# Kernel tuning notes

Hardware: AMD Instinct MI355X
Metric: run time of the kernel (lower is better)

Reference implementation:

```python
import jax, jax.numpy as jnp
import numpy as np

D_MODEL = 512
N_HEADS = 8
D_HEAD = D_MODEL // N_HEADS
N_BINS = 32


def setup_inputs() -> dict:
    key = jax.random.key(0)
    ks = jax.random.split(key, 12)
    B, N = 8, 1024
    x = jax.random.normal(ks[0], (B, N, D_MODEL), dtype=jnp.float32)
    positions = jax.random.randint(ks[1], (B, N), 0, 5000, dtype=jnp.int32)
    mask = jnp.ones((B, N), dtype=jnp.float32)
    s = 0.02
    qw = jax.random.normal(ks[2], (D_MODEL, D_MODEL), jnp.float32) * s
    qb = jnp.zeros((D_MODEL,), jnp.float32)
    kw = jax.random.normal(ks[3], (D_MODEL, D_MODEL), jnp.float32) * s
    kb = jnp.zeros((D_MODEL,), jnp.float32)
    vw = jax.random.normal(ks[4], (D_MODEL, D_MODEL), jnp.float32) * s
    vb = jnp.zeros((D_MODEL,), jnp.float32)
    ow = jax.random.normal(ks[5], (D_MODEL, D_MODEL), jnp.float32) * s
    ob = jnp.zeros((D_MODEL,), jnp.float32)
    dist_emb = jax.random.normal(ks[6], (N_BINS, N_HEADS), jnp.float32) * s
    order_bias = jnp.zeros((N_HEADS,), jnp.float32)
    bin_edges = jnp.logspace(0.0, 3.0, N_BINS - 1, dtype=jnp.float32)
    return {"x": x, "positions": positions, "mask": mask,
            "qw": qw, "qb": qb, "kw": kw, "kb": kb, "vw": vw, "vb": vb,
            "ow": ow, "ob": ob, "dist_emb": dist_emb, "order_bias": order_bias,
            "bin_edges": bin_edges}


def reference(x, positions, mask, qw, qb, kw, kb, vw, vb, ow, ob, dist_emb, order_bias, bin_edges):
    B, N, _ = x.shape
    scale = jnp.sqrt(jnp.float32(D_HEAD))
    # projections (torch Linear: y = x @ W^T + b), split heads -> (B,H,N,Dh)
    q = (x @ qw.T + qb).reshape(B, N, N_HEADS, D_HEAD).transpose(0, 2, 1, 3)
    k = (x @ kw.T + kb).reshape(B, N, N_HEADS, D_HEAD).transpose(0, 2, 1, 3)
    v = (x @ vw.T + vb).reshape(B, N, N_HEADS, D_HEAD).transpose(0, 2, 1, 3)
    scores = jnp.einsum('bhqd,bhkd->bhqk', q, k) / scale  # (B,H,N,N)
    pos = positions.astype(jnp.float32)
    pos_i = pos[:, :, None]   # (B,N,1)
    pos_j = pos[:, None, :]   # (B,1,N)
    dist = jnp.abs(pos_j - pos_i)  # (B,N,N)
    # torch.bucketize(right=False) == searchsorted side='left'
    bins = jnp.clip(jnp.searchsorted(bin_edges, dist, side='left'), 0, N_BINS - 1)
    dist_bias = dist_emb[bins]  # (B,N,N,H)
    scores = scores + dist_bias.transpose(0, 3, 1, 2)
    order_sign = (pos_j > pos_i).astype(scores.dtype) - 0.5  # (B,N,N)
    scores = scores + order_sign[:, None, :, :] * order_bias[None, :, None, None]
    mask_2d = mask[:, None, None, :] * mask[:, None, :, None]  # (B,1,N,N)
    scores = jnp.where(mask_2d == 0, jnp.float32(-1e9), scores)
    attn = jax.nn.softmax(scores, axis=-1)
    attn = jnp.nan_to_num(attn, nan=0.0)
    out = jnp.einsum('bhqk,bhkd->bhqd', attn, v)
    out = out.transpose(0, 2, 1, 3).reshape(B, N, D_MODEL)
    out = out * mask[..., None]
    return out @ ow.T + ob
```

## Files before the change

### kernel.cpp

```cpp
#include <hip/hip_runtime.h>
#include <hip/hip_bf16.h>

#define SEQ   1024
#define NH    8
#define DH    64

typedef __attribute__((ext_vector_type(8))) _Float16 half8;
typedef __attribute__((ext_vector_type(4))) _Float16 half4;
typedef __attribute__((ext_vector_type(4))) float    f32x4;

#if __has_builtin(__builtin_amdgcn_exp2f)
#define EXP2F __builtin_amdgcn_exp2f
#else
#define EXP2F exp2f
#endif

__device__ inline unsigned pk2(float a, float b) {
  return __builtin_bit_cast(unsigned, __builtin_amdgcn_cvt_pkrtz(a, b));
}
__device__ inline void swap32(unsigned &a, unsigned &b) {
  asm("v_permlane32_swap_b32 %0, %1" : "+v"(a), "+v"(b));
}
__device__ inline void swap16(unsigned &a, unsigned &b) {
  asm("v_permlane16_swap_b32 %0, %1" : "+v"(a), "+v"(b));
}
__device__ inline half8 mk8(unsigned a, unsigned b, unsigned c, unsigned d) {
  union { unsigned u[4]; half8 h; } x;
  x.u[0] = a; x.u[1] = b; x.u[2] = c; x.u[3] = d;
  return x.h;
}
__device__ __forceinline__ void gload16(const _Float16* g, _Float16* l) {
  __builtin_amdgcn_global_load_lds((const __attribute__((address_space(1))) void*)g,
                                   (__attribute__((address_space(3))) void*)l, 16, 0, 0);
}

#define BARRIER1 do {                                        \
    __builtin_amdgcn_sched_barrier(0);                       \
    asm volatile("s_waitcnt vmcnt(1)" ::: "memory");         \
    __builtin_amdgcn_s_barrier();                            \
    __builtin_amdgcn_sched_barrier(0);                       \
  } while (0)

__global__ void prep_all(const float* __restrict__ x,
                         const float* __restrict__ qw, const float* __restrict__ kw,
                         const float* __restrict__ vw, const float* __restrict__ ow,
                         const float* __restrict__ qb, const float* __restrict__ kb,
                         const float* __restrict__ vb, const float* __restrict__ edges,
                         _Float16* __restrict__ xh, _Float16* __restrict__ wqkvh,
                         _Float16* __restrict__ owh, float* __restrict__ qkvbias,
                         unsigned char* __restrict__ lutd) {
  const int blk = blockIdx.x, tid = threadIdx.x;
  if (blk < 4096) {
    int g = blk * 256 + tid;
    float4 v = reinterpret_cast<const float4*>(x)[g];
    half4 u;
    u[0] = (_Float16)v.x; u[1] = (_Float16)v.y; u[2] = (_Float16)v.z; u[3] = (_Float16)v.w;
    reinterpret_cast<half4*>(xh)[g] = u;
  } else if (blk < 5122) {
    int g = (blk - 4096) * 256 + tid;
    if (g < 196608) {
      const float* src = (g < 65536) ? qw : (g < 131072) ? kw : vw;
      int lg = g & 65535;
      float4 v = reinterpret_cast<const float4*>(src)[lg];
      half4 u;
      u[0] = (_Float16)v.x; u[1] = (_Float16)v.y; u[2] = (_Float16)v.z; u[3] = (_Float16)v.w;
      reinterpret_cast<half4*>(wqkvh)[g] = u;
    } else if (g < 262144) {
      int lg = g - 196608;
      float4 v = reinterpret_cast<const float4*>(ow)[lg];
      half4 u;
      u[0] = (_Float16)v.x; u[1] = (_Float16)v.y; u[2] = (_Float16)v.z; u[3] = (_Float16)v.w;
      reinterpret_cast<half4*>(owh)[lg] = u;
    } else if (g < 262528) {
      int lg = g - 262144;
      const float* src = (lg < 128) ? qb : (lg < 256) ? kb : vb;
      int ll = lg & 127;
      reinterpret_cast<float4*>(qkvbias)[lg] = reinterpret_cast<const float4*>(src)[ll];
    }
  } else {
    int d = (blk - 5122) * 256 + tid;
    float fd = (float)d;
    int bin = 0;
#pragma unroll
    for (int t = 0; t < 31; ++t) bin += (edges[t] < fd) ? 1 : 0;
    lutd[d] = (unsigned char)bin;
  }
}

__global__ __launch_bounds__(256) void prep_ebins(const int* __restrict__ positions,
                                                  const float* __restrict__ mask,
                                                  const unsigned char* __restrict__ lutd,
                                                  unsigned char* __restrict__ ebins) {
  __shared__ unsigned char lutl[5120];
  __shared__ int posl[SEQ];
  __shared__ unsigned char mk[SEQ];
  const int b = blockIdx.x >> 8, j0 = (blockIdx.x & 255) * 4;
  const int tid = threadIdx.x;
  for (int i = tid; i < 1280; i += 256)
    reinterpret_cast<unsigned*>(lutl)[i] = reinterpret_cast<const unsigned*>(lutd)[i];
  for (int i = tid; i < SEQ; i += 256) {
    posl[i] = positions[b * SEQ + i];
    mk[i] = (mask[b * SEQ + i] == 0.f) ? 32 : 0;
  }
  __syncthreads();
  const int c0 = tid * 4;
  const int widx = (tid >> 4) * 16 + (tid & 3) * 4 + ((tid >> 2) & 3);
#pragma unroll
  for (int jj = 0; jj < 4; ++jj) {
    const int j = j0 + jj;
    const int pr = posl[j];
    unsigned out = 0;
#pragma unroll
    for (int r = 0; r < 4; ++r) {
      int c = c0 + r;
      int pc = posl[c];
      int d = pc - pr; d = d < 0 ? -d : d;
      if (d > 5119) d = 5119;
      unsigned e = lutl[d] | (unsigned)mk[c] | ((pc > pr) ? 64u : 0u);
      out |= e << (8 * r);
    }
    reinterpret_cast<unsigned*>(&ebins[(size_t)(b * SEQ + j) * SEQ])[widx] = out;
  }
}

__global__ __launch_bounds__(256) void qkv_gemm3(const _Float16* __restrict__ xh,
                                                 const _Float16* __restrict__ wh,
                                                 const float* __restrict__ bias,
                                                 _Float16* __restrict__ qkv) {
  __shared__ __attribute__((aligned(16))) _Float16 As[128 * 64];
  __shared__ __attribute__((aligned(16))) _Float16 Bs[128 * 64];
  const int m0 = blockIdx.x * 128, n0 = blockIdx.y * 128;
  const int tid = threadIdx.x, w = tid >> 6, lane = tid & 63;
  const int lr = lane & 15, lg = lane >> 4;
  const int wr = (w >> 1) * 64, wc = (w & 1) * 64;
  f32x4 acc[4][4] = {};
  const int srow8 = lane >> 3;
  const int scol = ((lane & 7) ^ srow8) * 8;
  for (int k0 = 0; k0 < 512; k0 += 64) {
#pragma unroll
    for (int j = 0; j < 4; ++j) {
      const int row = (w * 4 + j) * 8 + srow8;
      gload16(&xh[(size_t)(m0 + row) * 512 + k0 + scol], &As[(w * 4 + j) * 512]);
      gload16(&wh[(size_t)(n0 + row) * 512 + k0 + scol], &Bs[(w * 4 + j) * 512]);
    }
    __syncthreads();
#pragma unroll
    for (int kk = 0; kk < 2; ++kk) {
      half8 af[4], bf[4];
#pragma unroll
      for (int mt = 0; mt < 4; ++mt) {
        const int row = wr + mt * 16 + lr;
        af[mt] = *reinterpret_cast<const half8*>(
            (const char*)As + row * 128 + (((kk * 4 + lg) ^ (row & 7)) * 16));
      }
#pragma unroll
      for (int nt = 0; nt < 4; ++nt) {
        const int row = wc + nt * 16 + lr;
        bf[nt] = *reinterpret_cast<const half8*>(
            (const char*)Bs + row * 128 + (((kk * 4 + lg) ^ (row & 7)) * 16));
      }
#pragma unroll
      for (int mt = 0; mt < 4; ++mt)
#pragma unroll
        for (int nt = 0; nt < 4; ++nt)
          acc[mt][nt] = __builtin_amdgcn_mfma_f32_16x16x32_f16(af[mt], bf[nt], acc[mt][nt], 0, 0, 0);
    }
    __syncthreads();
  }
  const int p = n0 >> 9;
  const float scl = (p == 0) ? 0.125f : (p == 1) ? 1.44269504f : 1.0f;
  if (p < 2) {
#pragma unroll
    for (int nt = 0; nt < 4; ++nt) {
      int n = n0 + wc + nt * 16 + lr;
      float bv = bias[n];
      int c = n & 511, h = c >> 6, d = c & 63;
#pragma unroll
      for (int mt = 0; mt < 4; ++mt)
#pragma unroll
        for (int r = 0; r < 4; ++r) {
          int m = m0 + wr + mt * 16 + lg * 4 + r;
          int bb = m >> 10, nn = m & 1023;
          qkv[p * 4194304 + ((bb * NH + h) * SEQ + nn) * DH + d] = (_Float16)((acc[mt][nt][r] + bv) * scl);
        }
    }
  } else {
#pragma unroll
    for (int nt = 0; nt < 4; ++nt) {
      int n = n0 + wc + nt * 16 + lr;
      float bv = bias[n];
      int c = n & 511, h = c >> 6, d = c & 63;
#pragma unroll
      for (int mt = 0; mt < 4; ++mt) {
        int m = m0 + wr + mt * 16 + lg * 4;
        int bb = m >> 10, nn = m & 1023;
        half4 st;
#pragma unroll
        for (int r = 0; r < 4; ++r) st[r] = (_Float16)(acc[mt][nt][r] + bv);
        *reinterpret_cast<half4*>(&qkv[8388608 + ((bb * NH + h) * DH + d) * SEQ + nn]) = st;
      }
    }
  }
}

#define ASTAGE(bufi, kv0_) do {                                                              \
    _Pragma("unroll") for (int j = 0; j < 2; ++j) {                                          \
      const int row_ = (w * 2 + j) * 8 + (lane >> 3);                                        \
      const int c_ = ((lane & 7) ^ (row_ & 7)) * 8;                                          \
      gload16(Kg + (size_t)((kv0_) + row_) * 64 + c_, &KsL + (bufi) * 4096 + (w * 2 + j) * 512); \
      gload16(Vtg + (size_t)row_ * 1024 + (kv0_) + c_, &VtL + (bufi) * 4096 + (w * 2 + j) * 512); \
    }                                                                                        \
  } while (0)

#define EBL(dst, kt_) do {                                                                   \
    uint4 e4_ = *reinterpret_cast<const uint4*>(ebrow + (kt_) * 64);                         \
    dst[0] = e4_.x; dst[1] = e4_.y; dst[2] = e4_.z; dst[3] = e4_.w;                          \
  } while (0)

#define ACOMP(bufi, ebw) do {                                                                \
    f32x4 s[4];                                                                              \
    _Pragma("unroll") for (int ct = 0; ct < 4; ++ct) {                                       \
      const unsigned eb_ = ebw[ct];                                                          \
      s[ct][0] = elut3[eb_ & 127u];                                                          \
      s[ct][1] = elut3[(eb_ >> 8) & 127u];                                                   \
      s[ct][2] = elut3[(eb_ >> 16) & 127u];                                                  \
      s[ct][3] = elut3[(eb_ >> 24) & 127u];                                                  \
    }                                                                                        \
    __builtin_amdgcn_s_setprio(1);                                                           \
    _Pragma("unroll") for (int ct = 0; ct < 4; ++ct) {                                       \
      half8 kf0 = *reinterpret_cast<const half8*>(ksbase + (bufi) * 8192 + koff[ct * 2 + 0]); \
      half8 kf1 = *reinterpret_cast<const half8*>(ksbase + (bufi) * 8192 + koff[ct * 2 + 1]); \
      s[ct] = __builtin_amdgcn_mfma_f32_16x16x32_f16(kf0, qf[0], s[ct], 0, 0, 0);            \
      s[ct] = __builtin_amdgcn_mfma_f32_16x16x32_f16(kf1, qf[1], s[ct], 0, 0, 0);            \
    }                                                                                        \
    __builtin_amdgcn_s_setprio(0);                                                           \
                 \
    unsigned W[4][2];                                                                        \
    _Pragma("unroll") for (int ct = 0; ct < 4; ++ct) {                                       \
      float p0 = EXP2F(s[ct][0]), p1 = EXP2F(s[ct][1]);                                      \
      float p2 = EXP2F(s[ct][2]), p3 = EXP2F(s[ct][3]);                                      \
      l_run += (p0 + p1) + (p2 + p3);                                                        \
      W[ct][0] = pk2(p0, p1);                                                                \
      W[ct][1] = pk2(p2, p3);                                                                \
    }                                                                                        \
    swap32(W[0][0], W[1][0]); swap32(W[0][1], W[1][1]);                                      \
    swap32(W[2][0], W[3][0]); swap32(W[2][1], W[3][1]);                                      \
    swap16(W[0][0], W[1][0]); swap16(W[0][1], W[1][1]);                                      \
    swap16(W[2][0], W[3][0]); swap16(W[2][1], W[3][1]);                                      \
    __builtin_amdgcn_s_setprio(1);                                                           \
    _Pragma("unroll") for (int ks = 0; ks < 2; ++ks) {                                       \
      half8 pa = mk8(W[ks * 2][0], W[ks * 2][1], W[ks * 2 + 1][0], W[ks * 2 + 1][1]);        \
      _Pragma("unroll") for (int dt = 0; dt < 4; ++dt) {                                     \
        half8 vf = *reinterpret_cast<const half8*>(vtbase + (bufi) * 8192 + voff[dt * 2 + ks]); \
        o[dt] = __builtin_amdgcn_mfma_f32_16x16x32_f16(vf, pa, o[dt], 0, 0, 0);              \
      }                                                                                      \
    }                                                                                        \
    __builtin_amdgcn_s_setprio(0);                                                           \
  } while (0)

__global__ __launch_bounds__(256, 4) void attn13(const _Float16* __restrict__ qkv,
                                                 const float* __restrict__ mask,
                                                 const unsigned char* __restrict__ ebins,
                                                 const float* __restrict__ demb,
                                                 const float* __restrict__ obias,
                                                 _Float16* __restrict__ aout) {
  __shared__ __attribute__((aligned(16))) _Float16 Ks[2][64 * 64];
  __shared__ __attribute__((aligned(16))) _Float16 Vt[2][64 * 64];
  __shared__ float elut3[128];

  const int blk = blockIdx.x;
  const int lin = (blk & 7) * 128 + (blk >> 3);
  const int qt = lin & 15, h = (lin >> 4) & 7, b = lin >> 7;
  const int tid = threadIdx.x, w = tid >> 6, lane = tid & 63;
  const int lr = lane & 15, lg = lane >> 4;

  const float obh = 0.5f * obias[h] * 1.44269504f;
  if (tid < 128) {
    float v;
    if (tid & 32) v = -1.442695e9f;
    else v = demb[(tid & 31) * NH + h] * 1.44269504f + ((tid & 64) ? obh : -obh);
    elut3[tid] = v;
  }

  const _Float16* Qg  = qkv + (size_t)(b * NH + h) * 65536;
  const _Float16* Kg  = qkv + 4194304 + (size_t)(b * NH + h) * 65536;
  const _Float16* Vtg = qkv + 8388608 + (size_t)(b * NH + h) * 65536;

  const int q_base = qt * 64 + w * 16;
  half8 qf[2];
#pragma unroll
  for (int ks = 0; ks < 2; ++ks)
    qf[ks] = *reinterpret_cast<const half8*>(&Qg[(q_base + lr) * DH + ks * 32 + lg * 8]);
  const float mq = mask[b * SEQ + q_base + lr];
  const unsigned char* ebrow = &ebins[(size_t)(b * SEQ + q_base + lr) * SEQ + lg * 16];

  _Float16& KsL = Ks[0][0];
  _Float16& VtL = Vt[0][0];
  const char* ksbase = (const char*)&Ks[0][0];
  const char* vtbase = (const char*)&Vt[0][0];
  int koff[8], voff[8];
#pragma unroll
  for (int ct = 0; ct < 4; ++ct) {
    const int krow = ct * 16 + lr;
    koff[ct * 2 + 0] = krow * 128 + (((0 + lg) ^ (krow & 7)) * 16);
    koff[ct * 2 + 1] = krow * 128 + (((4 + lg) ^ (krow & 7)) * 16);
    voff[ct * 2 + 0] = koff[ct * 2 + 0];
    voff[ct * 2 + 1] = koff[ct * 2 + 1];
  }

  float l_run = 0.f;
  f32x4 o[4] = {};

  unsigned ebwA[4], ebwB[4];
  ASTAGE(0, 0);
  EBL(ebwA, 0);
  __syncthreads();

#pragma unroll 1
  for (int i = 0; i < 8; ++i) {
    const int kt = 2 * i;
    ASTAGE(1, (kt + 1) * 64);
    EBL(ebwB, kt + 1);
    ACOMP(0, ebwA);
    BARRIER1;
    if (kt + 2 < 16) {
      ASTAGE(0, (kt + 2) * 64);
      EBL(ebwA, kt + 2);
    }
    ACOMP(1, ebwB);
    BARRIER1;
  }

  float s_ = l_run;
  s_ += __shfl_xor(s_, 16);
  s_ += __shfl_xor(s_, 32);
  const float linv = mq / fmaxf(s_, 1e-35f);
#pragma unroll
  for (int dt = 0; dt < 4; ++dt) {
    half4 st;
#pragma unroll
    for (int r = 0; r < 4; ++r) st[r] = (_Float16)(o[dt][r] * linv);
    *reinterpret_cast<half4*>(
        &aout[(size_t)(b * SEQ + q_base + lr) * 512 + h * DH + dt * 16 + lg * 4]) = st;
  }
}

__global__ __launch_bounds__(256) void out_gemm3(const _Float16* __restrict__ ah,
                                                 const _Float16* __restrict__ wh,
                                                 const float* __restrict__ ob,
                                                 float* __restrict__ out) {
  __shared__ __attribute__((aligned(16))) _Float16 As[128 * 64];
  __shared__ __attribute__((aligned(16))) _Float16 Bs[64 * 64];
  const int m0 = blockIdx.x * 128, n0 = blockIdx.y * 64;
  const int tid = threadIdx.x, w = tid >> 6, lane = tid & 63;
  const int lr = lane & 15, lg = lane >> 4;
  const int wr = (w >> 1) * 64, wc = (w & 1) * 32;
  f32x4 acc[4][2] = {};
  const int srow8 = lane >> 3;
  const int scol = ((lane & 7) ^ srow8) * 8;
  for (int k0 = 0; k0 < 512; k0 += 64) {
#pragma unroll
    for (int j = 0; j < 4; ++j) {
      const int row = (w * 4 + j) * 8 + srow8;
      gload16(&ah[(size_t)(m0 + row) * 512 + k0 + scol], &As[(w * 4 + j) * 512]);
    }
#pragma unroll
    for (int j = 0; j < 2; ++j) {
      const int row = (w * 2 + j) * 8 + srow8;
      gload16(&wh[(size_t)(n0 + row) * 512 + k0 + scol], &Bs[(w * 2 + j) * 512]);
    }
    __syncthreads();
#pragma unroll
    for (int kk = 0; kk < 2; ++kk) {
      half8 af[4], bf[2];
#pragma unroll
      for (int mt = 0; mt < 4; ++mt) {
        const int row = wr + mt * 16 + lr;
        af[mt] = *reinterpret_cast<const half8*>(
            (const char*)As + row * 128 + (((kk * 4 + lg) ^ (row & 7)) * 16));
      }
#pragma unroll
      for (int nt = 0; nt < 2; ++nt) {
        const int row = wc + nt * 16 + lr;
        bf[nt] = *reinterpret_cast<const half8*>(
            (const char*)Bs + row * 128 + (((kk * 4 + lg) ^ (row & 7)) * 16));
      }
#pragma unroll
      for (int mt = 0; mt < 4; ++mt)
#pragma unroll
        for (int nt = 0; nt < 2; ++nt)
          acc[mt][nt] = __builtin_amdgcn_mfma_f32_16x16x32_f16(af[mt], bf[nt], acc[mt][nt], 0, 0, 0);
    }
    __syncthreads();
  }
#pragma unroll
  for (int nt = 0; nt < 2; ++nt) {
    int n = n0 + wc + nt * 16 + lr;
    float bv = ob[n];
#pragma unroll
    for (int mt = 0; mt < 4; ++mt)
#pragma unroll
      for (int r = 0; r < 4; ++r) {
        int m = m0 + wr + mt * 16 + lg * 4 + r;
        out[m * 512 + n] = acc[mt][nt][r] + bv;
      }
  }
}

extern "C" void kernel_launch(void* const* d_in, const int* in_sizes, int n_in,
                              void* d_out, int out_size, void* d_ws, size_t ws_size,
                              hipStream_t stream) {
  const float* x         = (const float*)d_in[0];
  const int*   positions = (const int*)d_in[1];
  const float* mask      = (const float*)d_in[2];
  const float* qw        = (const float*)d_in[3];
  const float* qb        = (const float*)d_in[4];
  const float* kw        = (const float*)d_in[5];
  const float* kb        = (const float*)d_in[6];
  const float* vw        = (const float*)d_in[7];
  const float* vb        = (const float*)d_in[8];
  const float* ow        = (const float*)d_in[9];
  const float* ob        = (const float*)d_in[10];
  const float* demb      = (const float*)d_in[11];
  const float* obias     = (const float*)d_in[12];
  const float* edges     = (const float*)d_in[13];

  char* ws = (char*)d_ws;
  _Float16* xh        = (_Float16*)(ws);
  unsigned char* ebins = (unsigned char*)(ws);
  _Float16* qkv       = (_Float16*)(ws + 8388608);
  _Float16* aouth     = (_Float16*)(ws + 33554432);
  _Float16* wqkvh     = (_Float16*)(ws + 41943040);
  _Float16* owh       = (_Float16*)(ws + 43515904);
  float*    qkvbias   = (float*)(ws + 44040192);
  unsigned char* lutd = (unsigned char*)(ws + 44046336);
  float*    outp      = (float*)d_out;

  prep_all<<<5142, 256, 0, stream>>>(x, qw, kw, vw, ow, qb, kb, vb, edges,
                                     xh, wqkvh, owh, qkvbias, lutd);
  qkv_gemm3<<<dim3(64, 12), 256, 0, stream>>>(xh, wqkvh, qkvbias, qkv);
  prep_ebins<<<2048, 256, 0, stream>>>(positions, mask, lutd, ebins);
  attn13<<<1024, 256, 0, stream>>>(qkv, mask, ebins, demb, obias, aouth);
  out_gemm3<<<dim3(64, 8), 256, 0, stream>>>(aouth, owh, ob, outp);
}
```

Measured before the change: 90.48 us.

## Process two query sub-tiles per wave to reuse K/V fragments in attention

Each wave now handles 32 query rows (two 16-row sub-tiles) instead of 16, so every K and V fragment read from LDS feeds two MFMAs. The block's query tile grows to 128, halving the grid to 512 blocks and halving total K/V staging traffic. The vmcnt wait count is raised to match the extra ebins load. In exchange, register pressure doubles for the accumulators (launch bounds drop to 2 blocks per SIMD), and 512 blocks may leave parts of the GPU underfilled.

```diff
diff --git a/kernel.cpp b/kernel.cpp
--- a/kernel.cpp
+++ b/kernel.cpp
@@ -34,9 +34,9 @@
                                    (__attribute__((address_space(3))) void*)l, 16, 0, 0);
 }
 
-#define BARRIER1 do {                                        \
+#define BARRIER2 do {                                        \
     __builtin_amdgcn_sched_barrier(0);                       \
-    asm volatile("s_waitcnt vmcnt(1)" ::: "memory");         \
+    asm volatile("s_waitcnt vmcnt(2)" ::: "memory");         \
     __builtin_amdgcn_s_barrier();                            \
     __builtin_amdgcn_sched_barrier(0);                       \
   } while (0)
@@ -213,52 +213,61 @@
   } while (0)
 
 #define EBL(dst, kt_) do {                                                                   \
-    uint4 e4_ = *reinterpret_cast<const uint4*>(ebrow + (kt_) * 64);                         \
-    dst[0] = e4_.x; dst[1] = e4_.y; dst[2] = e4_.z; dst[3] = e4_.w;                          \
+    uint4 e0_ = *reinterpret_cast<const uint4*>(ebrow0 + (kt_) * 64);                        \
+    uint4 e1_ = *reinterpret_cast<const uint4*>(ebrow1 + (kt_) * 64);                        \
+    dst[0][0] = e0_.x; dst[0][1] = e0_.y; dst[0][2] = e0_.z; dst[0][3] = e0_.w;              \
+    dst[1][0] = e1_.x; dst[1][1] = e1_.y; dst[1][2] = e1_.z; dst[1][3] = e1_.w;              \
   } while (0)
 
 #define ACOMP(bufi, ebw) do {                                                                \
-    f32x4 s[4];                                                                              \
-    _Pragma("unroll") for (int ct = 0; ct < 4; ++ct) {                                       \
-      const unsigned eb_ = ebw[ct];                                                          \
-      s[ct][0] = elut3[eb_ & 127u];                                                          \
-      s[ct][1] = elut3[(eb_ >> 8) & 127u];                                                   \
-      s[ct][2] = elut3[(eb_ >> 16) & 127u];                                                  \
-      s[ct][3] = elut3[(eb_ >> 24) & 127u];                                                  \
-    }                                                                                        \
+    f32x4 s[4][2];                                                                           \
+    _Pragma("unroll") for (int qc = 0; qc < 2; ++qc)                                         \
+      _Pragma("unroll") for (int ct = 0; ct < 4; ++ct) {                                     \
+        const unsigned eb_ = ebw[qc][ct];                                                    \
+        s[ct][qc][0] = elut3[eb_ & 127u];                                                    \
+        s[ct][qc][1] = elut3[(eb_ >> 8) & 127u];                                             \
+        s[ct][qc][2] = elut3[(eb_ >> 16) & 127u];                                            \
+        s[ct][qc][3] = elut3[(eb_ >> 24) & 127u];                                            \
+      }                                                                                      \
     __builtin_amdgcn_s_setprio(1);                                                           \
     _Pragma("unroll") for (int ct = 0; ct < 4; ++ct) {                                       \
       half8 kf0 = *reinterpret_cast<const half8*>(ksbase + (bufi) * 8192 + koff[ct * 2 + 0]); \
       half8 kf1 = *reinterpret_cast<const half8*>(ksbase + (bufi) * 8192 + koff[ct * 2 + 1]); \
-      s[ct] = __builtin_amdgcn_mfma_f32_16x16x32_f16(kf0, qf[0], s[ct], 0, 0, 0);            \
-      s[ct] = __builtin_amdgcn_mfma_f32_16x16x32_f16(kf1, qf[1], s[ct], 0, 0, 0);            \
+      _Pragma("unroll") for (int qc = 0; qc < 2; ++qc) {                                     \
+        s[ct][qc] = __builtin_amdgcn_mfma_f32_16x16x32_f16(kf0, qf[qc][0], s[ct][qc], 0, 0, 0); \
+        s[ct][qc] = __builtin_amdgcn_mfma_f32_16x16x32_f16(kf1, qf[qc][1], s[ct][qc], 0, 0, 0); \
+      }                                                                                      \
     }                                                                                        \
     __builtin_amdgcn_s_setprio(0);                                                           \
                  \
-    unsigned W[4][2];                                                                        \
-    _Pragma("unroll") for (int ct = 0; ct < 4; ++ct) {                                       \
-      float p0 = EXP2F(s[ct][0]), p1 = EXP2F(s[ct][1]);                                      \
-      float p2 = EXP2F(s[ct][2]), p3 = EXP2F(s[ct][3]);                                      \
-      l_run += (p0 + p1) + (p2 + p3);                                                        \
-      W[ct][0] = pk2(p0, p1);                                                                \
-      W[ct][1] = pk2(p2, p3);                                                                \
+    unsigned W[2][4][2];                                                                     \
+    _Pragma("unroll") for (int qc = 0; qc < 2; ++qc) {                                       \
+      _Pragma("unroll") for (int ct = 0; ct < 4; ++ct) {                                     \
+        float p0 = EXP2F(s[ct][qc][0]), p1 = EXP2F(s[ct][qc][1]);                            \
+        float p2 = EXP2F(s[ct][qc][2]), p3 = EXP2F(s[ct][qc][3]);                            \
+        l_run[qc] += (p0 + p1) + (p2 + p3);                                                  \
+        W[qc][ct][0] = pk2(p0, p1);                                                          \
+        W[qc][ct][1] = pk2(p2, p3);                                                          \
+      }                                                                                      \
+      swap32(W[qc][0][0], W[qc][1][0]); swap32(W[qc][0][1], W[qc][1][1]);                    \
+      swap32(W[qc][2][0], W[qc][3][0]); swap32(W[qc][2][1], W[qc][3][1]);                    \
+      swap16(W[qc][0][0], W[qc][1][0]); swap16(W[qc][0][1], W[qc][1][1]);                    \
+      swap16(W[qc][2][0], W[qc][3][0]); swap16(W[qc][2][1], W[qc][3][1]);                    \
     }                                                                                        \
-    swap32(W[0][0], W[1][0]); swap32(W[0][1], W[1][1]);                                      \
-    swap32(W[2][0], W[3][0]); swap32(W[2][1], W[3][1]);                                      \
-    swap16(W[0][0], W[1][0]); swap16(W[0][1], W[1][1]);                                      \
-    swap16(W[2][0], W[3][0]); swap16(W[2][1], W[3][1]);                                      \
     __builtin_amdgcn_s_setprio(1);                                                           \
     _Pragma("unroll") for (int ks = 0; ks < 2; ++ks) {                                       \
-      half8 pa = mk8(W[ks * 2][0], W[ks * 2][1], W[ks * 2 + 1][0], W[ks * 2 + 1][1]);        \
+      half8 pa0 = mk8(W[0][ks * 2][0], W[0][ks * 2][1], W[0][ks * 2 + 1][0], W[0][ks * 2 + 1][1]); \
+      half8 pa1 = mk8(W[1][ks * 2][0], W[1][ks * 2][1], W[1][ks * 2 + 1][0], W[1][ks * 2 + 1][1]); \
       _Pragma("unroll") for (int dt = 0; dt < 4; ++dt) {                                     \
         half8 vf = *reinterpret_cast<const half8*>(vtbase + (bufi) * 8192 + voff[dt * 2 + ks]); \
-        o[dt] = __builtin_amdgcn_mfma_f32_16x16x32_f16(vf, pa, o[dt], 0, 0, 0);              \
+        o[dt][0] = __builtin_amdgcn_mfma_f32_16x16x32_f16(vf, pa0, o[dt][0], 0, 0, 0);       \
+        o[dt][1] = __builtin_amdgcn_mfma_f32_16x16x32_f16(vf, pa1, o[dt][1], 0, 0, 0);       \
       }                                                                                      \
     }                                                                                        \
     __builtin_amdgcn_s_setprio(0);                                                           \
   } while (0)
 
-__global__ __launch_bounds__(256, 4) void attn13(const _Float16* __restrict__ qkv,
+__global__ __launch_bounds__(256, 2) void attn14(const _Float16* __restrict__ qkv,
                                                  const float* __restrict__ mask,
                                                  const unsigned char* __restrict__ ebins,
                                                  const float* __restrict__ demb,
@@ -269,8 +278,8 @@
   __shared__ float elut3[128];
 
   const int blk = blockIdx.x;
-  const int lin = (blk & 7) * 128 + (blk >> 3);
-  const int qt = lin & 15, h = (lin >> 4) & 7, b = lin >> 7;
+  const int lin = (blk & 7) * 64 + (blk >> 3);
+  const int qt = lin & 7, h = (lin >> 3) & 7, b = lin >> 6;
   const int tid = threadIdx.x, w = tid >> 6, lane = tid & 63;
   const int lr = lane & 15, lg = lane >> 4;
 
@@ -286,13 +295,18 @@
   const _Float16* Kg  = qkv + 4194304 + (size_t)(b * NH + h) * 65536;
   const _Float16* Vtg = qkv + 8388608 + (size_t)(b * NH + h) * 65536;
 
-  const int q_base = qt * 64 + w * 16;
-  half8 qf[2];
-#pragma unroll
-  for (int ks = 0; ks < 2; ++ks)
-    qf[ks] = *reinterpret_cast<const half8*>(&Qg[(q_base + lr) * DH + ks * 32 + lg * 8]);
-  const float mq = mask[b * SEQ + q_base + lr];
-  const unsigned char* ebrow = &ebins[(size_t)(b * SEQ + q_base + lr) * SEQ + lg * 16];
+  const int q_base = qt * 128 + w * 32;
+  half8 qf[2][2];
+#pragma unroll
+  for (int qc = 0; qc < 2; ++qc)
+#pragma unroll
+    for (int ks = 0; ks < 2; ++ks)
+      qf[qc][ks] = *reinterpret_cast<const half8*>(&Qg[(q_base + qc * 16 + lr) * DH + ks * 32 + lg * 8]);
+  float mq[2];
+#pragma unroll
+  for (int qc = 0; qc < 2; ++qc) mq[qc] = mask[b * SEQ + q_base + qc * 16 + lr];
+  const unsigned char* ebrow0 = &ebins[(size_t)(b * SEQ + q_base + lr) * SEQ + lg * 16];
+  const unsigned char* ebrow1 = &ebins[(size_t)(b * SEQ + q_base + 16 + lr) * SEQ + lg * 16];
 
   _Float16& KsL = Ks[0][0];
   _Float16& VtL = Vt[0][0];
@@ -308,10 +322,10 @@
     voff[ct * 2 + 1] = koff[ct * 2 + 1];
   }
 
-  float l_run = 0.f;
-  f32x4 o[4] = {};
-
-  unsigned ebwA[4], ebwB[4];
+  float l_run[2] = {0.f, 0.f};
+  f32x4 o[4][2] = {};
+
+  unsigned ebwA[2][4], ebwB[2][4];
   ASTAGE(0, 0);
   EBL(ebwA, 0);
   __syncthreads();
@@ -322,27 +336,33 @@
     ASTAGE(1, (kt + 1) * 64);
     EBL(ebwB, kt + 1);
     ACOMP(0, ebwA);
-    BARRIER1;
+    BARRIER2;
     if (kt + 2 < 16) {
       ASTAGE(0, (kt + 2) * 64);
       EBL(ebwA, kt + 2);
     }
     ACOMP(1, ebwB);
-    BARRIER1;
-  }
-
-  float s_ = l_run;
-  s_ += __shfl_xor(s_, 16);
-  s_ += __shfl_xor(s_, 32);
-  const float linv = mq / fmaxf(s_, 1e-35f);
-#pragma unroll
-  for (int dt = 0; dt < 4; ++dt) {
-    half4 st;
-#pragma unroll
-    for (int r = 0; r < 4; ++r) st[r] = (_Float16)(o[dt][r] * linv);
-    *reinterpret_cast<half4*>(
-        &aout[(size_t)(b * SEQ + q_base + lr) * 512 + h * DH + dt * 16 + lg * 4]) = st;
-  }
+    BARRIER2;
+  }
+
+  float linv[2];
+#pragma unroll
+  for (int qc = 0; qc < 2; ++qc) {
+    float s_ = l_run[qc];
+    s_ += __shfl_xor(s_, 16);
+    s_ += __shfl_xor(s_, 32);
+    linv[qc] = mq[qc] / fmaxf(s_, 1e-35f);
+  }
+#pragma unroll
+  for (int dt = 0; dt < 4; ++dt)
+#pragma unroll
+    for (int qc = 0; qc < 2; ++qc) {
+      half4 st;
+#pragma unroll
+      for (int r = 0; r < 4; ++r) st[r] = (_Float16)(o[dt][qc][r] * linv[qc]);
+      *reinterpret_cast<half4*>(
+          &aout[(size_t)(b * SEQ + q_base + qc * 16 + lr) * 512 + h * DH + dt * 16 + lg * 4]) = st;
+    }
 }
 
 __global__ __launch_bounds__(256) void out_gemm3(const _Float16* __restrict__ ah,
@@ -440,6 +460,6 @@
                                      xh, wqkvh, owh, qkvbias, lutd);
   qkv_gemm3<<<dim3(64, 12), 256, 0, stream>>>(xh, wqkvh, qkvbias, qkv);
   prep_ebins<<<2048, 256, 0, stream>>>(positions, mask, lutd, ebins);
-  attn13<<<1024, 256, 0, stream>>>(qkv, mask, ebins, demb, obias, aouth);
+  attn14<<<512, 256, 0, stream>>>(qkv, mask, ebins, demb, obias, aouth);
   out_gemm3<<<dim3(64, 8), 256, 0, stream>>>(aouth, owh, ob, outp);
 }
```

Result: faster. 87.47 us, median of 2 (-3.3%).
